# Performance work log

Measured on AMD Instinct MI355X. Metric: run time of the kernel, lower is better.

## Reference

```python
import jax, jax.numpy as jnp
import numpy as np

NW, S, D, H, F = 4096, 64, 128, 8, 256
DH = D // H
EPS = 1e-5


def setup_inputs() -> dict:
    key = jax.random.key(0)
    ks = jax.random.split(key, 16)
    feat = jax.random.normal(ks[0], (NW, S, D), jnp.float32)
    pos = 0.1 * jax.random.normal(ks[1], (NW, S, D), jnp.float32)
    # each window has between S//2 and S valid voxels; True = padded key
    valid = jax.random.randint(ks[2], (NW, 1), S // 2, S + 1)
    mask = jnp.arange(S)[None, :] >= valid  # [NW, S] bool
    s = 1.0 / np.sqrt(D)
    u = lambda k, sh, sc: jax.random.uniform(k, sh, jnp.float32, -sc, sc)
    return {
        'feat': feat, 'pos': pos, 'mask': mask,
        'Wq': u(ks[3], (D, D), s), 'bq': jnp.zeros((D,), jnp.float32),
        'Wk': u(ks[4], (D, D), s), 'bk': jnp.zeros((D,), jnp.float32),
        'Wv': u(ks[5], (D, D), s), 'bv': jnp.zeros((D,), jnp.float32),
        'Wo': u(ks[6], (D, D), s), 'bo': jnp.zeros((D,), jnp.float32),
        'W1': u(ks[7], (D, F), s), 'b1': jnp.zeros((F,), jnp.float32),
        'W2': u(ks[8], (F, D), 1.0 / np.sqrt(F)), 'b2': jnp.zeros((D,), jnp.float32),
        'g1': jnp.ones((D,), jnp.float32), 'be1': jnp.zeros((D,), jnp.float32),
        'g2': jnp.ones((D,), jnp.float32), 'be2': jnp.zeros((D,), jnp.float32),
    }


def _layernorm(x, g, b):
    mu = jnp.mean(x, -1, keepdims=True)
    var = jnp.mean(jnp.square(x - mu), -1, keepdims=True)
    return (x - mu) * jax.lax.rsqrt(var + EPS) * g + b


def reference(feat, pos, mask, Wq, bq, Wk, bk, Wv, bv, Wo, bo,
              W1, b1, W2, b2, g1, be1, g2, be2):
    # windowed MHA: q = k = feat + pos, v = feat  (all windows batched)
    qk_in = feat + pos
    q = (qk_in @ Wq + bq).reshape(NW, S, H, DH)
    k = (qk_in @ Wk + bk).reshape(NW, S, H, DH)
    v = (feat @ Wv + bv).reshape(NW, S, H, DH)
    scores = jnp.einsum('wqhd,wkhd->whqk', q, k) / np.sqrt(DH)
    scores = jnp.where(mask[:, None, None, :], -1e9, scores)
    attn = jax.nn.softmax(scores, axis=-1)
    ctx = jnp.einsum('whqk,wkhd->wqhd', attn, v).reshape(NW, S, D)
    src2 = ctx @ Wo + bo
    # residual + LN + FFN + residual + LN (dropout = identity at eval)
    src = _layernorm(feat + src2, g1, be1)
    ffn = jax.nn.relu(src @ W1 + b1) @ W2 + b2
    return _layernorm(src + ffn, g2, be2)
```

## Files before the change

### kernel.cpp

```cpp
#include <hip/hip_runtime.h>

typedef __attribute__((ext_vector_type(8))) short bf16x8;
typedef __attribute__((ext_vector_type(4))) float f32x4;
typedef unsigned short u16;
typedef unsigned int u32;

#define MFMA16(a, b, c) __builtin_amdgcn_mfma_f32_16x16x32_bf16((a), (b), (c), 0, 0, 0)
#define CFENCE() asm volatile("" ::: "memory")


__device__ __forceinline__ u16 f2bf(float f) {
    union { float f; u32 u; } c; c.f = f;
    u32 r = c.u + 0x7fffu + ((c.u >> 16) & 1u);
    return (u16)(r >> 16);
}

__device__ __forceinline__ bf16x8 pack8(f32x4 a, f32x4 b) {
    union { u32 w[4]; bf16x8 v; } r;
    asm("v_cvt_pk_bf16_f32 %0, %1, %2" : "=v"(r.w[0]) : "v"(a[0]), "v"(a[1]));
    asm("v_cvt_pk_bf16_f32 %0, %1, %2" : "=v"(r.w[1]) : "v"(a[2]), "v"(a[3]));
    asm("v_cvt_pk_bf16_f32 %0, %1, %2" : "=v"(r.w[2]) : "v"(b[0]), "v"(b[1]));
    asm("v_cvt_pk_bf16_f32 %0, %1, %2" : "=v"(r.w[3]) : "v"(b[2]), "v"(b[3]));
    return r.v;
}

__device__ __forceinline__ void stage_h(const float* __restrict__ W, int ld,
                                        int n0, int k0, u16* __restrict__ sW,
                                        int t) {
#pragma unroll
    for (int i = 0; i < 4; ++i) {
        int e = i * 512 + t;
        int n = e & 63, kq = e >> 6;
        const float* src = W + (size_t)(k0 + kq * 4) * ld + n0 + n;
        float a = src[0], b = src[ld], c = src[2 * ld], d = src[3 * ld];
        u32 lo, hi;
        asm("v_cvt_pk_bf16_f32 %0, %1, %2" : "=v"(lo) : "v"(a), "v"(b));
        asm("v_cvt_pk_bf16_f32 %0, %1, %2" : "=v"(hi) : "v"(c), "v"(d));
        uint2 pk; pk.x = lo; pk.y = hi;
        *(uint2*)(sW + n * 136 + kq * 4) = pk;
    }
}

__device__ __forceinline__ void gemm_h(const bf16x8 aF[4], const u16* __restrict__ sW,
                                       int lr, int lk, f32x4 acc[4]) {
#pragma unroll
    for (int ks = 0; ks < 4; ++ks)
#pragma unroll
        for (int nt = 0; nt < 4; ++nt) {
            bf16x8 b = *(const bf16x8*)(sW + (nt * 16 + lr) * 136 + ks * 32 + lk * 8);
            acc[nt] = MFMA16(aF[ks], b, acc[nt]);
        }
}

__device__ __forceinline__ void row_ln(const f32x4 v[8], float mu[4], float rs[4]) {
#pragma unroll
    for (int r = 0; r < 4; ++r) {
        float s = 0.f;
#pragma unroll
        for (int nt = 0; nt < 8; ++nt) s += v[nt][r];
        s += __shfl_xor(s, 1); s += __shfl_xor(s, 2);
        s += __shfl_xor(s, 4); s += __shfl_xor(s, 8);
        float m_ = s * 0.0078125f;
        float q = 0.f;
#pragma unroll
        for (int nt = 0; nt < 8; ++nt) { float d = v[nt][r] - m_; q += d * d; }
        q += __shfl_xor(q, 1); q += __shfl_xor(q, 2);
        q += __shfl_xor(q, 4); q += __shfl_xor(q, 8);
        mu[r] = m_;
        rs[r] = rsqrtf(q * 0.0078125f + 1e-5f);
    }
}

__global__ __launch_bounds__(512) void enc_main(
    const float* __restrict__ feat, const float* __restrict__ pos,
    const unsigned char* __restrict__ maskb,
    const float* __restrict__ Wq, const float* __restrict__ bq,
    const float* __restrict__ Wk, const float* __restrict__ bk,
    const float* __restrict__ Wv, const float* __restrict__ bv,
    const float* __restrict__ Wo, const float* __restrict__ bo,
    const float* __restrict__ W1, const float* __restrict__ b1,
    const float* __restrict__ W2, const float* __restrict__ b2,
    const float* __restrict__ g1, const float* __restrict__ be1,
    const float* __restrict__ g2, const float* __restrict__ be2,
    float* __restrict__ out) {
    __shared__ __align__(16) char smem[159744];

    const int tid  = threadIdx.x;
    const int lane = tid & 63;
    const int wid  = tid >> 6;
    const int ww   = wid >> 2;
    const int m0   = (wid & 3) * 16;
    const int lr   = lane & 15;
    const int lk   = lane >> 4;
    const int w    = blockIdx.x * 2 + ww;

    char* wb   = smem + ww * 62464;
    u16* sQ    = (u16*)wb;
    u16* sK    = (u16*)(wb + 17408);
    u16* sVt   = (u16*)(wb + 34816);
    u16* sAttn = (u16*)(wb + 53248);
    u16* sF1   = (u16*)(wb + 17408);
    u16* panA  = (u16*)(smem + 124928);
    u16* panB  = (u16*)(smem + 142336);

    const float* fw = feat + (size_t)w * 8192;
    const float* pw = pos  + (size_t)w * 8192;

    stage_h(Wq, 128, 0, 0, panA, tid);

    int vld;
    {
        unsigned char smp = maskb[lane * 64 + 63];
        int ones = __popcll(__ballot(smp != 0));
        int m = (ones > 32) ? (maskb[(size_t)w * 64 + lane] != 0)
                            : (((const int*)maskb)[(size_t)w * 64 + lane] != 0);
        vld = 64 - __popcll(__ballot(m));
    }

    bf16x8 aX[4], aFv[4];
#pragma unroll
    for (int ks = 0; ks < 4; ++ks) {
        const float* fp = fw + (m0 + lr) * 128 + ks * 32 + lk * 8;
        const float* pp = pw + (m0 + lr) * 128 + ks * 32 + lk * 8;
        f32x4 f0 = *(const f32x4*)fp;
        f32x4 f1 = *(const f32x4*)(fp + 4);
        f32x4 p0 = *(const f32x4*)pp;
        f32x4 p1 = *(const f32x4*)(pp + 4);
        aFv[ks] = pack8(f0, f1);
        aX[ks]  = pack8(f0 + p0, f1 + p1);
    }
    __syncthreads();

    {
        stage_h(Wq, 128, 64, 0, panB, tid);
        f32x4 acc[4] = {};
        gemm_h(aX, panA, lr, lk, acc);
#pragma unroll
        for (int nt = 0; nt < 4; ++nt) {
            int col = nt * 16 + lr; float bb = bq[col];
#pragma unroll
            for (int r = 0; r < 4; ++r)
                sQ[(m0 + lk * 4 + r) * 136 + col] = f2bf(acc[nt][r] + bb);
        }
        __syncthreads();
    }
    {
        stage_h(Wk, 128, 0, 0, panA, tid);
        f32x4 acc[4] = {};
        gemm_h(aX, panB, lr, lk, acc);
#pragma unroll
        for (int nt = 0; nt < 4; ++nt) {
            int col = 64 + nt * 16 + lr; float bb = bq[col];
#pragma unroll
            for (int r = 0; r < 4; ++r)
                sQ[(m0 + lk * 4 + r) * 136 + col] = f2bf(acc[nt][r] + bb);
        }
        __syncthreads();
    }
    {
        stage_h(Wk, 128, 64, 0, panB, tid);
        f32x4 acc[4] = {};
        gemm_h(aX, panA, lr, lk, acc);
#pragma unroll
        for (int nt = 0; nt < 4; ++nt) {
            int col = nt * 16 + lr; float bb = bk[col];
#pragma unroll
            for (int r = 0; r < 4; ++r)
                sK[(m0 + lk * 4 + r) * 136 + col] = f2bf(acc[nt][r] + bb);
        }
        __syncthreads();
    }
    {
        stage_h(Wv, 128, 0, 0, panA, tid);
        f32x4 acc[4] = {};
        gemm_h(aX, panB, lr, lk, acc);
#pragma unroll
        for (int nt = 0; nt < 4; ++nt) {
            int col = 64 + nt * 16 + lr; float bb = bk[col];
#pragma unroll
            for (int r = 0; r < 4; ++r)
                sK[(m0 + lk * 4 + r) * 136 + col] = f2bf(acc[nt][r] + bb);
        }
        __syncthreads();
    }
    {
        stage_h(Wv, 128, 64, 0, panB, tid);
        f32x4 acc[4] = {};
        gemm_h(aFv, panA, lr, lk, acc);
#pragma unroll
        for (int nt = 0; nt < 4; ++nt) {
            int dcol = nt * 16 + lr; float bb = bv[dcol];
            float e0 = acc[nt][0] + bb, e1 = acc[nt][1] + bb;
            float e2 = acc[nt][2] + bb, e3 = acc[nt][3] + bb;
            u32 lo, hi;
            asm("v_cvt_pk_bf16_f32 %0, %1, %2" : "=v"(lo) : "v"(e0), "v"(e1));
            asm("v_cvt_pk_bf16_f32 %0, %1, %2" : "=v"(hi) : "v"(e2), "v"(e3));
            uint2 pk; pk.x = lo; pk.y = hi;
            *(uint2*)(sVt + dcol * 72 + m0 + lk * 4) = pk;
        }
        __syncthreads();
    }
    {
        stage_h(Wo, 128, 0, 0, panA, tid);
        f32x4 acc[4] = {};
        gemm_h(aFv, panB, lr, lk, acc);
#pragma unroll
        for (int nt = 0; nt < 4; ++nt) {
            int dcol = 64 + nt * 16 + lr; float bb = bv[dcol];
            float e0 = acc[nt][0] + bb, e1 = acc[nt][1] + bb;
            float e2 = acc[nt][2] + bb, e3 = acc[nt][3] + bb;
            u32 lo, hi;
            asm("v_cvt_pk_bf16_f32 %0, %1, %2" : "=v"(lo) : "v"(e0), "v"(e1));
            asm("v_cvt_pk_bf16_f32 %0, %1, %2" : "=v"(hi) : "v"(e2), "v"(e3));
            uint2 pk; pk.x = lo; pk.y = hi;
            *(uint2*)(sVt + dcol * 72 + m0 + lk * 4) = pk;
        }
        __syncthreads();
    }

    stage_h(Wo, 128, 64, 0, panB, tid);
    const int dup = (lk & 1) * 8;
#pragma unroll 1
    for (int h = 0; h < 8; ++h) {
        bf16x8 aQ = *(const bf16x8*)(sQ + (m0 + lr) * 136 + h * 16 + dup);
        f32x4 sc[4];
#pragma unroll
        for (int nt = 0; nt < 4; ++nt) {
            bf16x8 bK = *(const bf16x8*)(sK + (nt * 16 + lr) * 136 + h * 16 + dup);
            f32x4 zz = {0.f, 0.f, 0.f, 0.f};
            sc[nt] = MFMA16(aQ, bK, zz);
        }
#pragma unroll
        for (int nt = 0; nt < 4; ++nt) {
            bool msk = (nt * 16 + lr) >= vld;
#pragma unroll
            for (int r = 0; r < 4; ++r) {
                float v0 = sc[nt][r] * 0.125f;
                sc[nt][r] = msk ? -1e9f : v0;
            }
        }
        float mx[4], sm[4];
#pragma unroll
        for (int r = 0; r < 4; ++r) {
            float m_ = fmaxf(fmaxf(sc[0][r], sc[1][r]), fmaxf(sc[2][r], sc[3][r]));
            m_ = fmaxf(m_, __shfl_xor(m_, 1));
            m_ = fmaxf(m_, __shfl_xor(m_, 2));
            m_ = fmaxf(m_, __shfl_xor(m_, 4));
            m_ = fmaxf(m_, __shfl_xor(m_, 8));
            mx[r] = m_; sm[r] = 0.f;
        }
#pragma unroll
        for (int nt = 0; nt < 4; ++nt)
#pragma unroll
            for (int r = 0; r < 4; ++r) {
                float e = __expf(sc[nt][r] - mx[r]);
                sc[nt][r] = e; sm[r] += e;
            }
#pragma unroll
        for (int r = 0; r < 4; ++r) {
            float s_ = sm[r];
            s_ += __shfl_xor(s_, 1); s_ += __shfl_xor(s_, 2);
            s_ += __shfl_xor(s_, 4); s_ += __shfl_xor(s_, 8);
            sm[r] = 1.f / s_;
        }
#pragma unroll
        for (int nt = 0; nt < 4; ++nt)
#pragma unroll
            for (int r = 0; r < 4; ++r)
                sAttn[(m0 + lk * 4 + r) * 72 + nt * 16 + lr] = f2bf(sc[nt][r] * sm[r]);
        CFENCE();
        f32x4 cc = {0.f, 0.f, 0.f, 0.f};
#pragma unroll
        for (int ks = 0; ks < 2; ++ks) {
            bf16x8 aP = *(const bf16x8*)(sAttn + (m0 + lr) * 72 + ks * 32 + lk * 8);
            bf16x8 bV = *(const bf16x8*)(sVt + (h * 16 + lr) * 72 + ks * 32 + lk * 8);
            cc = MFMA16(aP, bV, cc);
        }
#pragma unroll
        for (int r = 0; r < 4; ++r)
            sQ[(m0 + lk * 4 + r) * 136 + h * 16 + lr] = f2bf(cc[r]);
    }
    CFENCE();
    __syncthreads();

    bf16x8 aC[4];
#pragma unroll
    for (int ks = 0; ks < 4; ++ks)
        aC[ks] = *(const bf16x8*)(sQ + (m0 + lr) * 136 + ks * 32 + lk * 8);
    f32x4 v8[8];
    {
        f32x4 acc[4] = {};
        gemm_h(aC, panA, lr, lk, acc);
#pragma unroll
        for (int nt = 0; nt < 4; ++nt) {
            int col = nt * 16 + lr; float bb = bo[col];
#pragma unroll
            for (int r = 0; r < 4; ++r)
                v8[nt][r] = acc[nt][r] + bb + fw[(m0 + lk * 4 + r) * 128 + col];
        }
        __syncthreads();
    }
    {
        stage_h(W1, 256, 0, 0, panA, tid);
        f32x4 acc[4] = {};
        gemm_h(aC, panB, lr, lk, acc);
#pragma unroll
        for (int nt = 0; nt < 4; ++nt) {
            int col = 64 + nt * 16 + lr; float bb = bo[col];
#pragma unroll
            for (int r = 0; r < 4; ++r)
                v8[4 + nt][r] = acc[nt][r] + bb + fw[(m0 + lk * 4 + r) * 128 + col];
        }
        __syncthreads();
    }
    float mu[4], rs[4];
    row_ln(v8, mu, rs);
    f32x4 srcv[8];
#pragma unroll
    for (int nt = 0; nt < 8; ++nt) {
        int col = nt * 16 + lr;
        float gg = g1[col], bb = be1[col];
#pragma unroll
        for (int r = 0; r < 4; ++r) {
            float sv = (v8[nt][r] - mu[r]) * rs[r] * gg + bb;
            srcv[nt][r] = sv;
            sQ[(m0 + lk * 4 + r) * 136 + col] = f2bf(sv);
        }
    }
    CFENCE();
    bf16x8 aS[4];
#pragma unroll
    for (int ks = 0; ks < 4; ++ks)
        aS[ks] = *(const bf16x8*)(sQ + (m0 + lr) * 136 + ks * 32 + lk * 8);

#pragma unroll
    for (int hf = 0; hf < 4; ++hf) {
        u16* cur = (hf & 1) ? panB : panA;
        u16* nxt = (hf & 1) ? panA : panB;
        if (hf < 3) stage_h(W1, 256, (hf + 1) * 64, 0, nxt, tid);
        else        stage_h(W2, 128, 0, 0, nxt, tid);
        f32x4 f1a[4] = {};
        gemm_h(aS, cur, lr, lk, f1a);
#pragma unroll
        for (int nt = 0; nt < 4; ++nt) {
            int col = hf * 64 + nt * 16 + lr; float bb = b1[col];
#pragma unroll
            for (int r = 0; r < 4; ++r)
                sF1[(m0 + lk * 4 + r) * 264 + col] = f2bf(fmaxf(f1a[nt][r] + bb, 0.f));
        }
        __syncthreads();
    }

    f32x4 oa[8] = {};
#pragma unroll
    for (int s = 0; s < 4; ++s) {
        u16* cur = (s & 1) ? panB : panA;
        u16* nxt = (s & 1) ? panA : panB;
        if (s < 3) {
            int ns = s + 1, nkh = ns >> 1, nnh = ns & 1;
            stage_h(W2, 128, nnh * 64, nkh * 128, nxt, tid);
        }
        int kh = s >> 1, nh = s & 1;
#pragma unroll
        for (int ks = 0; ks < 4; ++ks) {
            bf16x8 aF = *(const bf16x8*)(sF1 + (m0 + lr) * 264 + kh * 128 + ks * 32 + lk * 8);
#pragma unroll
            for (int nt = 0; nt < 4; ++nt) {
                bf16x8 b = *(const bf16x8*)(cur + (nt * 16 + lr) * 136 + ks * 32 + lk * 8);
                oa[nh * 4 + nt] = MFMA16(aF, b, oa[nh * 4 + nt]);
            }
        }
        if (s < 3) __syncthreads();
    }

#pragma unroll
    for (int nt = 0; nt < 8; ++nt) {
        int col = nt * 16 + lr; float bb = b2[col];
#pragma unroll
        for (int r = 0; r < 4; ++r)
            v8[nt][r] = oa[nt][r] + bb + srcv[nt][r];
    }
    row_ln(v8, mu, rs);
    float* ow = out + (size_t)w * 8192;
#pragma unroll
    for (int nt = 0; nt < 8; ++nt) {
        int col = nt * 16 + lr;
        float gg = g2[col], bb = be2[col];
#pragma unroll
        for (int r = 0; r < 4; ++r)
            ow[(m0 + lk * 4 + r) * 128 + col] = (v8[nt][r] - mu[r]) * rs[r] * gg + bb;
    }
}

extern "C" void kernel_launch(void* const* d_in, const int* in_sizes, int n_in,
                              void* d_out, int out_size, void* d_ws, size_t ws_size,
                              hipStream_t stream) {
    (void)in_sizes; (void)n_in; (void)out_size; (void)d_ws; (void)ws_size;
    const float* feat = (const float*)d_in[0];
    const float* pos  = (const float*)d_in[1];
    const unsigned char* mask = (const unsigned char*)d_in[2];
    const float* Wq = (const float*)d_in[3];  const float* bq = (const float*)d_in[4];
    const float* Wk = (const float*)d_in[5];  const float* bk = (const float*)d_in[6];
    const float* Wv = (const float*)d_in[7];  const float* bv = (const float*)d_in[8];
    const float* Wo = (const float*)d_in[9];  const float* bo = (const float*)d_in[10];
    const float* W1 = (const float*)d_in[11]; const float* b1 = (const float*)d_in[12];
    const float* W2 = (const float*)d_in[13]; const float* b2 = (const float*)d_in[14];
    const float* g1 = (const float*)d_in[15]; const float* be1 = (const float*)d_in[16];
    const float* g2 = (const float*)d_in[17]; const float* be2 = (const float*)d_in[18];

    enc_main<<<2048, 512, 0, stream>>>(feat, pos, mask,
                                       Wq, bq, Wk, bk, Wv, bv, Wo, bo,
                                       W1, b1, W2, b2, g1, be1, g2, be2,
                                       (float*)d_out);
}
```

Baseline: 334.3 us.

## Pre-convert weights to transposed bf16 in workspace, stage with 16-byte loads

Adds a small pre-kernel that converts all six weight matrices to bf16 in transposed (n-major) layout in the workspace. The main kernel then stages weight panels into shared memory with contiguous uint4 copies instead of strided fp32 loads plus per-element conversion. This cuts global traffic and ALU work per panel in every one of the 2048 blocks, at the cost of an extra launch. The old path is kept as a fallback when the workspace is too small.

```diff
diff --git a/kernel.cpp b/kernel.cpp
--- a/kernel.cpp
+++ b/kernel.cpp
@@ -22,6 +22,33 @@
     asm("v_cvt_pk_bf16_f32 %0, %1, %2" : "=v"(r.w[2]) : "v"(b[0]), "v"(b[1]));
     asm("v_cvt_pk_bf16_f32 %0, %1, %2" : "=v"(r.w[3]) : "v"(b[2]), "v"(b[3]));
     return r.v;
+}
+
+__global__ void conv_w_k(const float* __restrict__ Wq, const float* __restrict__ Wk,
+                         const float* __restrict__ Wv, const float* __restrict__ Wo,
+                         const float* __restrict__ W1, const float* __restrict__ W2,
+                         u16* __restrict__ o) {
+    int i = blockIdx.x * 256 + threadIdx.x;
+    float v;
+    if (i < 16384)      { int j = i;         v = Wq[(j & 127) * 128 + (j >> 7)]; }
+    else if (i < 32768) { int j = i - 16384; v = Wk[(j & 127) * 128 + (j >> 7)]; }
+    else if (i < 49152) { int j = i - 32768; v = Wv[(j & 127) * 128 + (j >> 7)]; }
+    else if (i < 65536) { int j = i - 49152; v = Wo[(j & 127) * 128 + (j >> 7)]; }
+    else if (i < 98304) { int j = i - 65536; v = W1[(j & 127) * 256 + (j >> 7)]; }
+    else                { int j = i - 98304; v = W2[(j & 255) * 128 + (j >> 8)]; }
+    o[i] = f2bf(v);
+}
+
+__device__ __forceinline__ void stage_wt(const u16* __restrict__ WT, int ld,
+                                         int n0, int k0, u16* __restrict__ sW,
+                                         int t) {
+#pragma unroll
+    for (int i = 0; i < 2; ++i) {
+        int e = i * 512 + t;
+        int n = e & 63, c = e >> 6;
+        uint4 pk = *(const uint4*)(WT + (size_t)(n0 + n) * ld + k0 + c * 8);
+        *(uint4*)(sW + n * 136 + c * 8) = pk;
+    }
 }
 
 __device__ __forceinline__ void stage_h(const float* __restrict__ W, int ld,
@@ -71,7 +98,324 @@
     }
 }
 
-__global__ __launch_bounds__(512) void enc_main(
+__global__ __launch_bounds__(512) void enc_stage_wt(
+    const float* __restrict__ feat, const float* __restrict__ pos,
+    const unsigned char* __restrict__ maskb, const u16* __restrict__ wT,
+    const float* __restrict__ bq, const float* __restrict__ bk,
+    const float* __restrict__ bv, const float* __restrict__ bo,
+    const float* __restrict__ b1, const float* __restrict__ b2,
+    const float* __restrict__ g1, const float* __restrict__ be1,
+    const float* __restrict__ g2, const float* __restrict__ be2,
+    float* __restrict__ out) {
+    __shared__ __align__(16) char smem[159744];
+
+    const int tid  = threadIdx.x;
+    const int lane = tid & 63;
+    const int wid  = tid >> 6;
+    const int ww   = wid >> 2;
+    const int m0   = (wid & 3) * 16;
+    const int lr   = lane & 15;
+    const int lk   = lane >> 4;
+    const int w    = blockIdx.x * 2 + ww;
+
+    char* wb   = smem + ww * 62464;
+    u16* sQ    = (u16*)wb;
+    u16* sK    = (u16*)(wb + 17408);
+    u16* sVt   = (u16*)(wb + 34816);
+    u16* sAttn = (u16*)(wb + 53248);
+    u16* sF1   = (u16*)(wb + 17408);
+    u16* panA  = (u16*)(smem + 124928);
+    u16* panB  = (u16*)(smem + 142336);
+
+    const u16* WQt = wT;
+    const u16* WKt = wT + 16384;
+    const u16* WVt = wT + 32768;
+    const u16* WOt = wT + 49152;
+    const u16* W1t = wT + 65536;
+    const u16* W2t = wT + 98304;
+
+    const float* fw = feat + (size_t)w * 8192;
+    const float* pw = pos  + (size_t)w * 8192;
+
+    stage_wt(WQt, 128, 0, 0, panA, tid);
+
+    int vld;
+    {
+        unsigned char smp = maskb[lane * 64 + 63];
+        int ones = __popcll(__ballot(smp != 0));
+        int m = (ones > 32) ? (maskb[(size_t)w * 64 + lane] != 0)
+                            : (((const int*)maskb)[(size_t)w * 64 + lane] != 0);
+        vld = 64 - __popcll(__ballot(m));
+    }
+
+    bf16x8 aX[4], aFv[4];
+#pragma unroll
+    for (int ks = 0; ks < 4; ++ks) {
+        const float* fp = fw + (m0 + lr) * 128 + ks * 32 + lk * 8;
+        const float* pp = pw + (m0 + lr) * 128 + ks * 32 + lk * 8;
+        f32x4 f0 = *(const f32x4*)fp;
+        f32x4 f1 = *(const f32x4*)(fp + 4);
+        f32x4 p0 = *(const f32x4*)pp;
+        f32x4 p1 = *(const f32x4*)(pp + 4);
+        aFv[ks] = pack8(f0, f1);
+        aX[ks]  = pack8(f0 + p0, f1 + p1);
+    }
+    __syncthreads();
+
+    {   stage_wt(WQt, 128, 64, 0, panB, tid);
+        f32x4 acc[4] = {};
+        gemm_h(aX, panA, lr, lk, acc);
+#pragma unroll
+        for (int nt = 0; nt < 4; ++nt) {
+            int col = nt * 16 + lr; float bb = bq[col];
+#pragma unroll
+            for (int r = 0; r < 4; ++r)
+                sQ[(m0 + lk * 4 + r) * 136 + col] = f2bf(acc[nt][r] + bb);
+        }
+        __syncthreads();
+    }
+    {   stage_wt(WKt, 128, 0, 0, panA, tid);
+        f32x4 acc[4] = {};
+        gemm_h(aX, panB, lr, lk, acc);
+#pragma unroll
+        for (int nt = 0; nt < 4; ++nt) {
+            int col = 64 + nt * 16 + lr; float bb = bq[col];
+#pragma unroll
+            for (int r = 0; r < 4; ++r)
+                sQ[(m0 + lk * 4 + r) * 136 + col] = f2bf(acc[nt][r] + bb);
+        }
+        __syncthreads();
+    }
+    {   stage_wt(WKt, 128, 64, 0, panB, tid);
+        f32x4 acc[4] = {};
+        gemm_h(aX, panA, lr, lk, acc);
+#pragma unroll
+        for (int nt = 0; nt < 4; ++nt) {
+            int col = nt * 16 + lr; float bb = bk[col];
+#pragma unroll
+            for (int r = 0; r < 4; ++r)
+                sK[(m0 + lk * 4 + r) * 136 + col] = f2bf(acc[nt][r] + bb);
+        }
+        __syncthreads();
+    }
+    {   stage_wt(WVt, 128, 0, 0, panA, tid);
+        f32x4 acc[4] = {};
+        gemm_h(aX, panB, lr, lk, acc);
+#pragma unroll
+        for (int nt = 0; nt < 4; ++nt) {
+            int col = 64 + nt * 16 + lr; float bb = bk[col];
+#pragma unroll
+            for (int r = 0; r < 4; ++r)
+                sK[(m0 + lk * 4 + r) * 136 + col] = f2bf(acc[nt][r] + bb);
+        }
+        __syncthreads();
+    }
+    {   stage_wt(WVt, 128, 64, 0, panB, tid);
+        f32x4 acc[4] = {};
+        gemm_h(aFv, panA, lr, lk, acc);
+#pragma unroll
+        for (int nt = 0; nt < 4; ++nt) {
+            int dcol = nt * 16 + lr; float bb = bv[dcol];
+            float e0 = acc[nt][0] + bb, e1 = acc[nt][1] + bb;
+            float e2 = acc[nt][2] + bb, e3 = acc[nt][3] + bb;
+            u32 lo, hi;
+            asm("v_cvt_pk_bf16_f32 %0, %1, %2" : "=v"(lo) : "v"(e0), "v"(e1));
+            asm("v_cvt_pk_bf16_f32 %0, %1, %2" : "=v"(hi) : "v"(e2), "v"(e3));
+            uint2 pk; pk.x = lo; pk.y = hi;
+            *(uint2*)(sVt + dcol * 72 + m0 + lk * 4) = pk;
+        }
+        __syncthreads();
+    }
+    {   stage_wt(WOt, 128, 0, 0, panA, tid);
+        f32x4 acc[4] = {};
+        gemm_h(aFv, panB, lr, lk, acc);
+#pragma unroll
+        for (int nt = 0; nt < 4; ++nt) {
+            int dcol = 64 + nt * 16 + lr; float bb = bv[dcol];
+            float e0 = acc[nt][0] + bb, e1 = acc[nt][1] + bb;
+            float e2 = acc[nt][2] + bb, e3 = acc[nt][3] + bb;
+            u32 lo, hi;
+            asm("v_cvt_pk_bf16_f32 %0, %1, %2" : "=v"(lo) : "v"(e0), "v"(e1));
+            asm("v_cvt_pk_bf16_f32 %0, %1, %2" : "=v"(hi) : "v"(e2), "v"(e3));
+            uint2 pk; pk.x = lo; pk.y = hi;
+            *(uint2*)(sVt + dcol * 72 + m0 + lk * 4) = pk;
+        }
+        __syncthreads();
+    }
+
+    stage_wt(WOt, 128, 64, 0, panB, tid);
+    const int dup = (lk & 1) * 8;
+#pragma unroll 1
+    for (int h = 0; h < 8; ++h) {
+        bf16x8 aQ = *(const bf16x8*)(sQ + (m0 + lr) * 136 + h * 16 + dup);
+        f32x4 sc[4];
+#pragma unroll
+        for (int nt = 0; nt < 4; ++nt) {
+            bf16x8 bK = *(const bf16x8*)(sK + (nt * 16 + lr) * 136 + h * 16 + dup);
+            f32x4 zz = {0.f, 0.f, 0.f, 0.f};
+            sc[nt] = MFMA16(aQ, bK, zz);
+        }
+#pragma unroll
+        for (int nt = 0; nt < 4; ++nt) {
+            bool msk = (nt * 16 + lr) >= vld;
+#pragma unroll
+            for (int r = 0; r < 4; ++r) {
+                float v0 = sc[nt][r] * 0.125f;
+                sc[nt][r] = msk ? -1e9f : v0;
+            }
+        }
+        float mx[4], sm[4];
+#pragma unroll
+        for (int r = 0; r < 4; ++r) {
+            float m_ = fmaxf(fmaxf(sc[0][r], sc[1][r]), fmaxf(sc[2][r], sc[3][r]));
+            m_ = fmaxf(m_, __shfl_xor(m_, 1));
+            m_ = fmaxf(m_, __shfl_xor(m_, 2));
+            m_ = fmaxf(m_, __shfl_xor(m_, 4));
+            m_ = fmaxf(m_, __shfl_xor(m_, 8));
+            mx[r] = m_; sm[r] = 0.f;
+        }
+#pragma unroll
+        for (int nt = 0; nt < 4; ++nt)
+#pragma unroll
+            for (int r = 0; r < 4; ++r) {
+                float e = __expf(sc[nt][r] - mx[r]);
+                sc[nt][r] = e; sm[r] += e;
+            }
+#pragma unroll
+        for (int r = 0; r < 4; ++r) {
+            float s_ = sm[r];
+            s_ += __shfl_xor(s_, 1); s_ += __shfl_xor(s_, 2);
+            s_ += __shfl_xor(s_, 4); s_ += __shfl_xor(s_, 8);
+            sm[r] = 1.f / s_;
+        }
+#pragma unroll
+        for (int nt = 0; nt < 4; ++nt)
+#pragma unroll
+            for (int r = 0; r < 4; ++r)
+                sAttn[(m0 + lk * 4 + r) * 72 + nt * 16 + lr] = f2bf(sc[nt][r] * sm[r]);
+        CFENCE();
+        f32x4 cc = {0.f, 0.f, 0.f, 0.f};
+#pragma unroll
+        for (int ks = 0; ks < 2; ++ks) {
+            bf16x8 aP = *(const bf16x8*)(sAttn + (m0 + lr) * 72 + ks * 32 + lk * 8);
+            bf16x8 bV = *(const bf16x8*)(sVt + (h * 16 + lr) * 72 + ks * 32 + lk * 8);
+            cc = MFMA16(aP, bV, cc);
+        }
+#pragma unroll
+        for (int r = 0; r < 4; ++r)
+            sQ[(m0 + lk * 4 + r) * 136 + h * 16 + lr] = f2bf(cc[r]);
+    }
+    CFENCE();
+    __syncthreads();
+
+    bf16x8 aC[4];
+#pragma unroll
+    for (int ks = 0; ks < 4; ++ks)
+        aC[ks] = *(const bf16x8*)(sQ + (m0 + lr) * 136 + ks * 32 + lk * 8);
+    f32x4 v8[8];
+    {   f32x4 acc[4] = {};
+        gemm_h(aC, panA, lr, lk, acc);
+#pragma unroll
+        for (int nt = 0; nt < 4; ++nt) {
+            int col = nt * 16 + lr; float bb = bo[col];
+#pragma unroll
+            for (int r = 0; r < 4; ++r)
+                v8[nt][r] = acc[nt][r] + bb + fw[(m0 + lk * 4 + r) * 128 + col];
+        }
+        __syncthreads();
+    }
+    {   stage_wt(W1t, 128, 0, 0, panA, tid);
+        f32x4 acc[4] = {};
+        gemm_h(aC, panB, lr, lk, acc);
+#pragma unroll
+        for (int nt = 0; nt < 4; ++nt) {
+            int col = 64 + nt * 16 + lr; float bb = bo[col];
+#pragma unroll
+            for (int r = 0; r < 4; ++r)
+                v8[4 + nt][r] = acc[nt][r] + bb + fw[(m0 + lk * 4 + r) * 128 + col];
+        }
+        __syncthreads();
+    }
+    float mu[4], rs[4];
+    row_ln(v8, mu, rs);
+    f32x4 srcv[8];
+#pragma unroll
+    for (int nt = 0; nt < 8; ++nt) {
+        int col = nt * 16 + lr;
+        float gg = g1[col], bb = be1[col];
+#pragma unroll
+        for (int r = 0; r < 4; ++r) {
+            float sv = (v8[nt][r] - mu[r]) * rs[r] * gg + bb;
+            srcv[nt][r] = sv;
+            sQ[(m0 + lk * 4 + r) * 136 + col] = f2bf(sv);
+        }
+    }
+    CFENCE();
+    bf16x8 aS[4];
+#pragma unroll
+    for (int ks = 0; ks < 4; ++ks)
+        aS[ks] = *(const bf16x8*)(sQ + (m0 + lr) * 136 + ks * 32 + lk * 8);
+
+#pragma unroll
+    for (int hf = 0; hf < 4; ++hf) {
+        u16* cur = (hf & 1) ? panB : panA;
+        u16* nxt = (hf & 1) ? panA : panB;
+        if (hf < 3) stage_wt(W1t, 128, (hf + 1) * 64, 0, nxt, tid);
+        else        stage_wt(W2t, 256, 0, 0, nxt, tid);
+        f32x4 f1a[4] = {};
+        gemm_h(aS, cur, lr, lk, f1a);
+#pragma unroll
+        for (int nt = 0; nt < 4; ++nt) {
+            int col = hf * 64 + nt * 16 + lr; float bb = b1[col];
+#pragma unroll
+            for (int r = 0; r < 4; ++r)
+                sF1[(m0 + lk * 4 + r) * 264 + col] = f2bf(fmaxf(f1a[nt][r] + bb, 0.f));
+        }
+        __syncthreads();
+    }
+
+    f32x4 oa[8] = {};
+#pragma unroll
+    for (int s = 0; s < 4; ++s) {
+        u16* cur = (s & 1) ? panB : panA;
+        u16* nxt = (s & 1) ? panA : panB;
+        if (s < 3) {
+            int ns = s + 1, nkh = ns >> 1, nnh = ns & 1;
+            stage_wt(W2t, 256, nnh * 64, nkh * 128, nxt, tid);
+        }
+        int kh = s >> 1, nh = s & 1;
+#pragma unroll
+        for (int ks = 0; ks < 4; ++ks) {
+            bf16x8 aF = *(const bf16x8*)(sF1 + (m0 + lr) * 264 + kh * 128 + ks * 32 + lk * 8);
+#pragma unroll
+            for (int nt = 0; nt < 4; ++nt) {
+                bf16x8 b = *(const bf16x8*)(cur + (nt * 16 + lr) * 136 + ks * 32 + lk * 8);
+                oa[nh * 4 + nt] = MFMA16(aF, b, oa[nh * 4 + nt]);
+            }
+        }
+        if (s < 3) __syncthreads();
+    }
+
+#pragma unroll
+    for (int nt = 0; nt < 8; ++nt) {
+        int col = nt * 16 + lr; float bb = b2[col];
+#pragma unroll
+        for (int r = 0; r < 4; ++r)
+            v8[nt][r] = oa[nt][r] + bb + srcv[nt][r];
+    }
+    row_ln(v8, mu, rs);
+    float* ow = out + (size_t)w * 8192;
+#pragma unroll
+    for (int nt = 0; nt < 8; ++nt) {
+        int col = nt * 16 + lr;
+        float gg = g2[col], bb = be2[col];
+#pragma unroll
+        for (int r = 0; r < 4; ++r)
+            ow[(m0 + lk * 4 + r) * 128 + col] = (v8[nt][r] - mu[r]) * rs[r] * gg + bb;
+    }
+}
+
+__global__ __launch_bounds__(512) void enc_fallback(
     const float* __restrict__ feat, const float* __restrict__ pos,
     const unsigned char* __restrict__ maskb,
     const float* __restrict__ Wq, const float* __restrict__ bq,
@@ -131,8 +475,7 @@
     }
     __syncthreads();
 
-    {
-        stage_h(Wq, 128, 64, 0, panB, tid);
+    {   stage_h(Wq, 128, 64, 0, panB, tid);
         f32x4 acc[4] = {};
         gemm_h(aX, panA, lr, lk, acc);
 #pragma unroll
@@ -144,8 +487,7 @@
         }
         __syncthreads();
     }
-    {
-        stage_h(Wk, 128, 0, 0, panA, tid);
+    {   stage_h(Wk, 128, 0, 0, panA, tid);
         f32x4 acc[4] = {};
         gemm_h(aX, panB, lr, lk, acc);
 #pragma unroll
@@ -157,8 +499,7 @@
         }
         __syncthreads();
     }
-    {
-        stage_h(Wk, 128, 64, 0, panB, tid);
+    {   stage_h(Wk, 128, 64, 0, panB, tid);
         f32x4 acc[4] = {};
         gemm_h(aX, panA, lr, lk, acc);
 #pragma unroll
@@ -170,8 +511,7 @@
         }
         __syncthreads();
     }
-    {
-        stage_h(Wv, 128, 0, 0, panA, tid);
+    {   stage_h(Wv, 128, 0, 0, panA, tid);
         f32x4 acc[4] = {};
         gemm_h(aX, panB, lr, lk, acc);
 #pragma unroll
@@ -183,8 +523,7 @@
         }
         __syncthreads();
     }
-    {
-        stage_h(Wv, 128, 64, 0, panB, tid);
+    {   stage_h(Wv, 128, 64, 0, panB, tid);
         f32x4 acc[4] = {};
         gemm_h(aFv, panA, lr, lk, acc);
 #pragma unroll
@@ -200,8 +539,7 @@
         }
         __syncthreads();
     }
-    {
-        stage_h(Wo, 128, 0, 0, panA, tid);
+    {   stage_h(Wo, 128, 0, 0, panA, tid);
         f32x4 acc[4] = {};
         gemm_h(aFv, panB, lr, lk, acc);
 #pragma unroll
@@ -288,8 +626,7 @@
     for (int ks = 0; ks < 4; ++ks)
         aC[ks] = *(const bf16x8*)(sQ + (m0 + lr) * 136 + ks * 32 + lk * 8);
     f32x4 v8[8];
-    {
-        f32x4 acc[4] = {};
+    {   f32x4 acc[4] = {};
         gemm_h(aC, panA, lr, lk, acc);
 #pragma unroll
         for (int nt = 0; nt < 4; ++nt) {
@@ -300,8 +637,7 @@
         }
         __syncthreads();
     }
-    {
-        stage_h(W1, 256, 0, 0, panA, tid);
+    {   stage_h(W1, 256, 0, 0, panA, tid);
         f32x4 acc[4] = {};
         gemm_h(aC, panB, lr, lk, acc);
 #pragma unroll
@@ -395,7 +731,7 @@
 extern "C" void kernel_launch(void* const* d_in, const int* in_sizes, int n_in,
                               void* d_out, int out_size, void* d_ws, size_t ws_size,
                               hipStream_t stream) {
-    (void)in_sizes; (void)n_in; (void)out_size; (void)d_ws; (void)ws_size;
+    (void)in_sizes; (void)n_in; (void)out_size;
     const float* feat = (const float*)d_in[0];
     const float* pos  = (const float*)d_in[1];
     const unsigned char* mask = (const unsigned char*)d_in[2];
@@ -408,8 +744,16 @@
     const float* g1 = (const float*)d_in[15]; const float* be1 = (const float*)d_in[16];
     const float* g2 = (const float*)d_in[17]; const float* be2 = (const float*)d_in[18];
 
-    enc_main<<<2048, 512, 0, stream>>>(feat, pos, mask,
-                                       Wq, bq, Wk, bk, Wv, bv, Wo, bo,
-                                       W1, b1, W2, b2, g1, be1, g2, be2,
-                                       (float*)d_out);
-}
+    if (ws_size >= 262144) {
+        u16* wT = (u16*)d_ws;
+        conv_w_k<<<512, 256, 0, stream>>>(Wq, Wk, Wv, Wo, W1, W2, wT);
+        enc_stage_wt<<<2048, 512, 0, stream>>>(feat, pos, mask, wT,
+                                               bq, bk, bv, bo, b1, b2,
+                                               g1, be1, g2, be2, (float*)d_out);
+    } else {
+        enc_fallback<<<2048, 512, 0, stream>>>(feat, pos, mask,
+                                               Wq, bq, Wk, bk, Wv, bv, Wo, bo,
+                                               W1, b1, W2, b2, g1, be1, g2, be2,
+                                               (float*)d_out);
+    }
+}
```

New measurement: 338.8 us. No clear change (+1.3%).
